# Kernel optimization log

Hardware: AMD Instinct MI355X
Metric: run time of the kernel (lower is better)

## Reference

```python
import jax, jax.numpy as jnp
import numpy as np
import math

B, S, D, H = 4, 2048, 1024, 16
DK = D // H  # 64
THETA = 10000.0


def setup_inputs() -> dict:
    key = jax.random.key(0)
    ks = jax.random.split(key, 5)
    std = 0.02
    return {
        "x": jax.random.normal(ks[0], (B, S, D), dtype=jnp.float32),
        "Wq": jax.random.normal(ks[1], (D, D), dtype=jnp.float32) * std,
        "Wk": jax.random.normal(ks[2], (D, D), dtype=jnp.float32) * std,
        "Wv": jax.random.normal(ks[3], (D, D), dtype=jnp.float32) * std,
        "Wo": jax.random.normal(ks[4], (D, D), dtype=jnp.float32) * std / math.sqrt(2 * 12),
        "token_positions": jnp.arange(S, dtype=jnp.int32),
    }


def _rope(x, pos):
    # x: [B, H, S, DK]; pos: [S]. Interleaved-pair rotary embedding.
    inv_freq = THETA ** (-jnp.arange(0, DK, 2, dtype=jnp.float32) / DK)  # [DK/2]
    ang = pos.astype(jnp.float32)[:, None] * inv_freq[None, :]  # [S, DK/2]
    cos, sin = jnp.cos(ang), jnp.sin(ang)
    x1, x2 = x[..., 0::2], x[..., 1::2]  # [B, H, S, DK/2]
    r1 = x1 * cos - x2 * sin
    r2 = x1 * sin + x2 * cos
    return jnp.stack([r1, r2], axis=-1).reshape(x.shape)


def reference(x, Wq, Wk, Wv, Wo, token_positions):
    b, s, d = x.shape
    Q = x @ Wq
    K = x @ Wk
    V = x @ Wv
    # [B, S, D] -> [B, H, S, DK]
    def split(t):
        return t.reshape(b, s, H, DK).transpose(0, 2, 1, 3)
    Qh, Kh, Vh = split(Q), split(K), split(V)
    Qh = _rope(Qh, token_positions)
    Kh = _rope(Kh, token_positions)
    scores = jnp.einsum('bhqd,bhkd->bhqk', Qh, Kh) / math.sqrt(DK)
    causal = jnp.tril(jnp.ones((s, s), dtype=bool))
    scores = jnp.where(causal, scores, -jnp.inf)
    probs = jax.nn.softmax(scores, axis=-1)
    out = jnp.einsum('bhqk,bhkd->bhqd', probs, Vh)
    out = out.transpose(0, 2, 1, 3).reshape(b, s, d)
    return out @ Wo
```

## Files before the change

### kernel.cpp

```cpp
#include <hip/hip_runtime.h>

#define B_N 4
#define S_LEN 2048
#define D_MODEL 1024
#define N_HEAD 16
#define D_HEAD 64
#define M_ROWS (B_N * S_LEN)

typedef short bf16x8 __attribute__((ext_vector_type(8)));
typedef float f32x4 __attribute__((ext_vector_type(4)));

__device__ __forceinline__ unsigned short f2bf(float f) {
  union { float f; unsigned int u; } v; v.f = f;
  unsigned int r = v.u + 0x7FFFu + ((v.u >> 16) & 1u);
  return (unsigned short)(r >> 16);
}
__device__ __forceinline__ float bf2f(unsigned short u) {
  union { unsigned int u; float f; } v; v.u = ((unsigned int)u) << 16;
  return v.f;
}
__device__ __forceinline__ bf16x8 ld8(const unsigned short* p) {
  return *reinterpret_cast<const bf16x8*>(p);
}
__device__ __forceinline__ void glds16(const unsigned short* g, unsigned short* l) {
  __builtin_amdgcn_global_load_lds(
      (const __attribute__((address_space(1))) unsigned int*)g,
      (__attribute__((address_space(3))) unsigned int*)l, 16, 0, 0);
}

__global__ __launch_bounds__(256) void rope_tab_k(const int* __restrict__ pos,
                                                  float2* __restrict__ tab) {
  const int idx = blockIdx.x * 256 + threadIdx.x;
  const int s = idx >> 5;
  const int i = idx & 31;
  const float inv = exp2f(-(float)i * 0.41524101186092029f);
  const float ang = (float)pos[s] * inv;
  tab[idx] = make_float2(cosf(ang), sinf(ang));
}

__global__ __launch_bounds__(256) void cast_k(const float* __restrict__ X,
                                              unsigned short* __restrict__ Y) {
  const size_t i = ((size_t)blockIdx.x * 256 + threadIdx.x) * 8;
  const float4 a = *reinterpret_cast<const float4*>(X + i);
  const float4 b = *reinterpret_cast<const float4*>(X + i + 4);
  __align__(16) unsigned short v[8];
  v[0] = f2bf(a.x); v[1] = f2bf(a.y); v[2] = f2bf(a.z); v[3] = f2bf(a.w);
  v[4] = f2bf(b.x); v[5] = f2bf(b.y); v[6] = f2bf(b.z); v[7] = f2bf(b.w);
  *reinterpret_cast<uint4*>(Y + i) = *reinterpret_cast<const uint4*>(v);
}

__global__ __launch_bounds__(256) void wtrans_k(
    const float* __restrict__ W0, const float* __restrict__ W1,
    const float* __restrict__ W2, const float* __restrict__ W3,
    unsigned short* __restrict__ T0, unsigned short* __restrict__ T1,
    unsigned short* __restrict__ T2, unsigned short* __restrict__ T3) {
  const int z = blockIdx.z;
  const float* __restrict__ W = (z == 0) ? W0 : (z == 1) ? W1 : (z == 2) ? W2 : W3;
  unsigned short* __restrict__ T = (z == 0) ? T0 : (z == 1) ? T1 : (z == 2) ? T2 : T3;
  __shared__ __align__(16) unsigned short tile[64][72];
  const int kb = blockIdx.x * 64;
  const int nb = blockIdx.y * 64;
#pragma unroll
  for (int it = 0; it < 2; ++it) {
    const int chunk = it * 256 + threadIdx.x;
    const int r = chunk >> 3;
    const int c8 = (chunk & 7) * 8;
    const float* src = W + (size_t)(kb + r) * D_MODEL + nb + c8;
    const float4 a = *reinterpret_cast<const float4*>(src);
    const float4 b = *reinterpret_cast<const float4*>(src + 4);
    __align__(16) unsigned short v[8];
    v[0] = f2bf(a.x); v[1] = f2bf(a.y); v[2] = f2bf(a.z); v[3] = f2bf(a.w);
    v[4] = f2bf(b.x); v[5] = f2bf(b.y); v[6] = f2bf(b.z); v[7] = f2bf(b.w);
    *reinterpret_cast<uint4*>(&tile[r][c8]) = *reinterpret_cast<const uint4*>(v);
  }
  __syncthreads();
#pragma unroll
  for (int it = 0; it < 2; ++it) {
    const int chunk = it * 256 + threadIdx.x;
    const int n = chunk >> 3;
    const int k8 = (chunk & 7) * 8;
    __align__(16) unsigned short vals[8];
#pragma unroll
    for (int j = 0; j < 8; ++j) vals[j] = tile[k8 + j][n];
    *reinterpret_cast<uint4*>(T + (size_t)(nb + n) * D_MODEL + kb + k8) =
        *reinterpret_cast<const uint4*>(vals);
  }
}

__global__ __launch_bounds__(256) void gemm2_k(
    const unsigned short* __restrict__ A, const unsigned short* __restrict__ W,
    unsigned short* __restrict__ Qo, unsigned short* __restrict__ Ko,
    unsigned short* __restrict__ VTo, float* __restrict__ OF,
    const float2* __restrict__ tab, const int mode) {
  __shared__ __align__(16) unsigned short smem[4][64][68];
  unsigned short* As = &smem[0][0][0];
  unsigned short* Bs = As + 128 * 32;

  const int tid = threadIdx.x;
  const int lane = tid & 63;
  const int w = tid >> 6;
  const int l15 = lane & 15;
  const int l4 = lane >> 4;

  const int row0 = blockIdx.x * 128;
  const int col0 = blockIdx.y * 128;

  const int srow = w * 32 + (lane >> 2);
  const int scol = (lane & 3) * 8;
  const unsigned short* ga = A + (size_t)(row0 + srow) * D_MODEL + scol;
  const unsigned short* gb = W + (size_t)(col0 + srow) * D_MODEL + scol;
  unsigned short* la = &As[(w * 32) * 32];
  unsigned short* lb = &Bs[(w * 32) * 32];

  const int wrow = (w & 1) * 64;
  const int wcol = (w >> 1) * 64;

  f32x4 acc[4][4];
  const f32x4 fz = {0.f, 0.f, 0.f, 0.f};
#pragma unroll
  for (int m = 0; m < 4; ++m)
#pragma unroll
    for (int n = 0; n < 4; ++n) acc[m][n] = fz;

  for (int kb = 0; kb < D_MODEL; kb += 32) {
    glds16(ga + kb, la);
    glds16(ga + 16 * D_MODEL + kb, la + 16 * 32);
    glds16(gb + kb, lb);
    glds16(gb + 16 * D_MODEL + kb, lb + 16 * 32);
    __syncthreads();
    bf16x8 af[4], bfr[4];
#pragma unroll
    for (int m = 0; m < 4; ++m) af[m] = ld8(&As[(wrow + m * 16 + l15) * 32 + l4 * 8]);
#pragma unroll
    for (int n = 0; n < 4; ++n) bfr[n] = ld8(&Bs[(wcol + n * 16 + l15) * 32 + l4 * 8]);
#pragma unroll
    for (int m = 0; m < 4; ++m)
#pragma unroll
      for (int n = 0; n < 4; ++n)
        acc[m][n] = __builtin_amdgcn_mfma_f32_16x16x32_bf16(af[m], bfr[n], acc[m][n], 0, 0, 0);
    __syncthreads();
  }

  if (mode == 1) {
#pragma unroll
    for (int n = 0; n < 4; ++n) {
      const int gcol = col0 + wcol + n * 16 + l15;
#pragma unroll
      for (int m = 0; m < 4; ++m)
#pragma unroll
        for (int r = 0; r < 4; ++r)
          OF[(size_t)(row0 + wrow + m * 16 + l4 * 4 + r) * D_MODEL + gcol] = acc[m][n][r];
    }
    return;
  }

  unsigned short (*T)[68] = (unsigned short(*)[68]) & smem[w];
  const bool isV = (col0 >= 2048);
  if (!isV) {
#pragma unroll
    for (int m = 0; m < 4; ++m)
#pragma unroll
      for (int n = 0; n < 4; ++n)
#pragma unroll
        for (int r = 0; r < 4; ++r)
          T[m * 16 + l4 * 4 + r][n * 16 + l15] = f2bf(acc[m][n][r]);
  } else {
#pragma unroll
    for (int m = 0; m < 4; ++m)
#pragma unroll
      for (int n = 0; n < 4; ++n)
#pragma unroll
        for (int r = 0; r < 4; ++r)
          T[n * 16 + l15][m * 16 + l4 * 4 + r] = f2bf(acc[m][n][r]);
  }

  const int lr = lane >> 3;
  const int lc = lane & 7;
  if (!isV) {
    const bool isQ = (col0 < 1024);
    unsigned short* O = isQ ? Qo : Ko;
    const float qs = isQ ? 0.18033688011112042f : 1.0f;
    const int cbase = (col0 & 1023) + wcol;
#pragma unroll
    for (int rg = 0; rg < 8; ++rg) {
      const int trow = rg * 8 + lr;
      const int grow = row0 + wrow + trow;
      const int s = grow & (S_LEN - 1);
      const bf16x8 vv = ld8(&T[trow][lc * 8]);
      const float4 tA = *reinterpret_cast<const float4*>(&tab[s * 32 + lc * 4]);
      const float4 tB = *reinterpret_cast<const float4*>(&tab[s * 32 + lc * 4 + 2]);
      float x[8];
#pragma unroll
      for (int j = 0; j < 8; ++j) x[j] = bf2f((unsigned short)vv[j]);
      __align__(16) unsigned short o8[8];
      o8[0] = f2bf((x[0] * tA.x - x[1] * tA.y) * qs);
      o8[1] = f2bf((x[0] * tA.y + x[1] * tA.x) * qs);
      o8[2] = f2bf((x[2] * tA.z - x[3] * tA.w) * qs);
      o8[3] = f2bf((x[2] * tA.w + x[3] * tA.z) * qs);
      o8[4] = f2bf((x[4] * tB.x - x[5] * tB.y) * qs);
      o8[5] = f2bf((x[4] * tB.y + x[5] * tB.x) * qs);
      o8[6] = f2bf((x[6] * tB.z - x[7] * tB.w) * qs);
      o8[7] = f2bf((x[6] * tB.w + x[7] * tB.z) * qs);
      *reinterpret_cast<uint4*>(O + (size_t)grow * D_MODEL + cbase + lc * 8) =
          *reinterpret_cast<const uint4*>(o8);
    }
  } else {
    const int vc0 = (col0 - 2048) + wcol;
    const int h = vc0 >> 6;
    const int b = row0 >> 11;
    const int s0 = (row0 & (S_LEN - 1)) + wrow;
#pragma unroll
    for (int rg = 0; rg < 8; ++rg) {
      const int dk = rg * 8 + lr;
      const bf16x8 vv = ld8(&T[dk][lc * 8]);
      *reinterpret_cast<bf16x8*>(
          VTo + ((size_t)((b << 4) + h) * 64 + dk) * S_LEN + s0 + lc * 8) = vv;
    }
  }
}

__global__ __launch_bounds__(256) void attn3_k(
    const unsigned short* __restrict__ Q, const unsigned short* __restrict__ K,
    const unsigned short* __restrict__ VT, unsigned short* __restrict__ O) {
  const int pair = blockIdx.x;
  const int h = blockIdx.y;
  const int b = blockIdx.z;
  const int tid = threadIdx.x;
  const int w = tid >> 6;
  const int lane = tid & 63;
  const int l15 = lane & 15;
  const int l4 = lane >> 4;

  __shared__ __align__(16) unsigned short Ks[64][72];
  __shared__ __align__(16) unsigned short Vs[64][72];
  __shared__ __align__(16) unsigned short Ps[4][32][72];

  const f32x4 fz = {0.f, 0.f, 0.f, 0.f};
  const unsigned short* kbase = K + (size_t)b * S_LEN * D_MODEL + h * D_HEAD;
  const unsigned short* vbase = VT + (size_t)((b << 4) + h) * 64 * S_LEN;
  const int srcl = ((lane & 15) >> 2) << 4;
  const int lq = lane & 3;

  for (int half = 0; half < 2; ++half) {
    const int qt = half ? (15 - pair) : pair;
    const int qb = qt * 128;
    const int qw0 = qb + w * 32;

    bf16x8 qf[2][2];
#pragma unroll
    for (int t = 0; t < 2; ++t)
#pragma unroll
      for (int kc = 0; kc < 2; ++kc)
        qf[t][kc] = ld8(Q + (size_t)(b * S_LEN + qw0 + t * 16 + l15) * D_MODEL +
                        h * D_HEAD + kc * 32 + l4 * 8);

    f32x4 o[4][2];
#pragma unroll
    for (int d = 0; d < 4; ++d)
#pragma unroll
      for (int t = 0; t < 2; ++t) o[d][t] = fz;
    float lsum[2][4];
#pragma unroll
    for (int t = 0; t < 2; ++t)
#pragma unroll
      for (int r = 0; r < 4; ++r) lsum[t][r] = 0.f;

    const int nkt = qb / 64 + 2;
    for (int kt = 0; kt < nkt; ++kt) {
      const int kb0 = kt * 64;
#pragma unroll
      for (int it = 0; it < 2; ++it) {
        const int chunk = it * 256 + tid;
        const int rr = chunk >> 3;
        const int c8 = (chunk & 7) * 8;
        *reinterpret_cast<uint4*>(&Ks[rr][c8]) =
            *reinterpret_cast<const uint4*>(kbase + (size_t)(kb0 + rr) * D_MODEL + c8);
        *reinterpret_cast<uint4*>(&Vs[rr][c8]) =
            *reinterpret_cast<const uint4*>(vbase + (size_t)rr * S_LEN + kb0 + c8);
      }
      __syncthreads();

      if (kb0 <= qw0 + 31) {
        bf16x8 kf[4][2];
#pragma unroll
        for (int n = 0; n < 4; ++n)
#pragma unroll
          for (int kc = 0; kc < 2; ++kc)
            kf[n][kc] = ld8(&Ks[n * 16 + l15][kc * 32 + l4 * 8]);
        f32x4 s[2][4];
#pragma unroll
        for (int t = 0; t < 2; ++t)
#pragma unroll
          for (int n = 0; n < 4; ++n) {
            f32x4 a0 = __builtin_amdgcn_mfma_f32_16x16x32_bf16(qf[t][0], kf[n][0], fz, 0, 0, 0);
            s[t][n] = __builtin_amdgcn_mfma_f32_16x16x32_bf16(qf[t][1], kf[n][1], a0, 0, 0, 0);
          }

#pragma unroll
        for (int t = 0; t < 2; ++t) {
          const bool full = (kb0 + 63 <= qw0 + t * 16);
          if (full) {
#pragma unroll
            for (int r = 0; r < 4; ++r) {
              float su = lsum[t][r];
#pragma unroll
              for (int n = 0; n < 4; ++n) {
                const float e = exp2f(s[t][n][r]);
                s[t][n][r] = e;
                su += e;
              }
              lsum[t][r] = su;
            }
          } else {
#pragma unroll
            for (int r = 0; r < 4; ++r) {
              const int q = qw0 + t * 16 + l4 * 4 + r;
              float su = lsum[t][r];
#pragma unroll
              for (int n = 0; n < 4; ++n) {
                const int key = kb0 + n * 16 + l15;
                float e = exp2f(s[t][n][r]);
                e = (key <= q) ? e : 0.f;
                s[t][n][r] = e;
                su += e;
              }
              lsum[t][r] = su;
            }
          }
#pragma unroll
          for (int r = 0; r < 4; ++r)
#pragma unroll
            for (int n = 0; n < 4; ++n)
              Ps[w][t * 16 + l4 * 4 + r][n * 16 + l15] = f2bf(s[t][n][r]);
        }

        bf16x8 vf[4][2], pf[2][2];
#pragma unroll
        for (int d = 0; d < 4; ++d)
#pragma unroll
          for (int kc = 0; kc < 2; ++kc)
            vf[d][kc] = ld8(&Vs[d * 16 + l15][kc * 32 + l4 * 8]);
#pragma unroll
        for (int t = 0; t < 2; ++t)
#pragma unroll
          for (int kc = 0; kc < 2; ++kc)
            pf[t][kc] = ld8(&Ps[w][t * 16 + l15][kc * 32 + l4 * 8]);
#pragma unroll
        for (int d = 0; d < 4; ++d)
#pragma unroll
          for (int t = 0; t < 2; ++t) {
            o[d][t] = __builtin_amdgcn_mfma_f32_16x16x32_bf16(vf[d][0], pf[t][0], o[d][t], 0, 0, 0);
            o[d][t] = __builtin_amdgcn_mfma_f32_16x16x32_bf16(vf[d][1], pf[t][1], o[d][t], 0, 0, 0);
          }
      }
      __syncthreads();
    }

#pragma unroll
    for (int t = 0; t < 2; ++t) {
#pragma unroll
      for (int dd = 1; dd < 16; dd <<= 1)
#pragma unroll
        for (int r = 0; r < 4; ++r) lsum[t][r] += __shfl_xor(lsum[t][r], dd);
      const float b0 = __shfl(lsum[t][0], srcl), b1 = __shfl(lsum[t][1], srcl);
      const float b2 = __shfl(lsum[t][2], srcl), b3 = __shfl(lsum[t][3], srcl);
      const float lv = (lq == 0) ? b0 : (lq == 1) ? b1 : (lq == 2) ? b2 : b3;
      const float li = 1.0f / lv;
      unsigned short* op = O + (size_t)(b * S_LEN + qw0 + t * 16 + l15) * D_MODEL +
                           h * D_HEAD + l4 * 4;
#pragma unroll
      for (int d = 0; d < 4; ++d) {
        ushort4 u;
        u.x = f2bf(o[d][t][0] * li); u.y = f2bf(o[d][t][1] * li);
        u.z = f2bf(o[d][t][2] * li); u.w = f2bf(o[d][t][3] * li);
        *reinterpret_cast<ushort4*>(op + d * 16) = u;
      }
    }
  }
}

extern "C" void kernel_launch(void* const* d_in, const int* in_sizes, int n_in,
                              void* d_out, int out_size, void* d_ws, size_t ws_size,
                              hipStream_t stream) {
  const float* x  = (const float*)d_in[0];
  const float* Wq = (const float*)d_in[1];
  const float* Wk = (const float*)d_in[2];
  const float* Wv = (const float*)d_in[3];
  const float* Wo = (const float*)d_in[4];
  const int* pos  = (const int*)d_in[5];
  float* out = (float*)d_out;

  char* ws = (char*)d_ws;
  const size_t big = (size_t)M_ROWS * D_MODEL * 2;
  const size_t wsz = (size_t)D_MODEL * D_MODEL * 2;
  unsigned short* xb  = (unsigned short*)(ws + 0 * big);
  unsigned short* Qb  = (unsigned short*)(ws + 1 * big);
  unsigned short* Kb  = (unsigned short*)(ws + 2 * big);
  unsigned short* VT  = (unsigned short*)(ws + 3 * big);
  unsigned short* Wqkvt = (unsigned short*)(ws + 4 * big);
  unsigned short* Wot   = (unsigned short*)(ws + 4 * big + 3 * wsz);
  float2* tab = (float2*)d_out;

  rope_tab_k<<<dim3(S_LEN * 32 / 256), 256, 0, stream>>>(pos, tab);
  cast_k<<<dim3(M_ROWS * D_MODEL / 2048), 256, 0, stream>>>(x, xb);
  wtrans_k<<<dim3(16, 16, 4), 256, 0, stream>>>(
      Wq, Wk, Wv, Wo, Wqkvt, Wqkvt + (size_t)D_MODEL * D_MODEL,
      Wqkvt + 2 * (size_t)D_MODEL * D_MODEL, Wot);
  gemm2_k<<<dim3(M_ROWS / 128, 3 * D_MODEL / 128), 256, 0, stream>>>(
      xb, Wqkvt, Qb, Kb, VT, nullptr, tab, 0);
  attn3_k<<<dim3(8, N_HEAD, B_N), 256, 0, stream>>>(Qb, Kb, VT, Qb);
  gemm2_k<<<dim3(M_ROWS / 128, D_MODEL / 128), 256, 0, stream>>>(
      Qb, Wot, nullptr, nullptr, nullptr, out, nullptr, 1);
}
```

Measured before the change: 296.6 us.

## Keep attention probabilities in registers and prefetch K/V tiles

The attention kernel computes S transposed (K as the A operand), so each lane holds four consecutive keys for one query row. Those probabilities are packed directly into bf16x4 operands for 16x16x16 MFMA, which removes the per-wave LDS round trip for P and shrinks the row-sum reduction to two shuffles. K/V tiles for the next step are now prefetched into registers while the current tile is computed. Float-to-bf16 conversions everywhere switch to the packed hardware intrinsic. The cost is more register pressure, and the smaller MFMA shape issues more instructions.

```diff
diff --git a/kernel.cpp b/kernel.cpp
--- a/kernel.cpp
+++ b/kernel.cpp
@@ -1,4 +1,5 @@
 #include <hip/hip_runtime.h>
+#include <hip/hip_bf16.h>
 
 #define B_N 4
 #define S_LEN 2048
@@ -8,7 +9,14 @@
 #define M_ROWS (B_N * S_LEN)
 
 typedef short bf16x8 __attribute__((ext_vector_type(8)));
+typedef short bf16x4 __attribute__((ext_vector_type(4)));
 typedef float f32x4 __attribute__((ext_vector_type(4)));
+
+#if __has_builtin(__builtin_amdgcn_mfma_f32_16x16x16bf16_1k)
+#define HAVE_MFMA16 1
+#else
+#define HAVE_MFMA16 0
+#endif
 
 __device__ __forceinline__ unsigned short f2bf(float f) {
   union { float f; unsigned int u; } v; v.f = f;
@@ -19,8 +27,16 @@
   union { unsigned int u; float f; } v; v.u = ((unsigned int)u) << 16;
   return v.f;
 }
+__device__ __forceinline__ unsigned int pkbf(float a, float b) {
+  union { __hip_bfloat162 h; unsigned int u; } cv;
+  cv.h = __float22bfloat162_rn(make_float2(a, b));
+  return cv.u;
+}
 __device__ __forceinline__ bf16x8 ld8(const unsigned short* p) {
   return *reinterpret_cast<const bf16x8*>(p);
+}
+__device__ __forceinline__ bf16x4 ld4(const unsigned short* p) {
+  return *reinterpret_cast<const bf16x4*>(p);
 }
 __device__ __forceinline__ void glds16(const unsigned short* g, unsigned short* l) {
   __builtin_amdgcn_global_load_lds(
@@ -43,10 +59,10 @@
   const size_t i = ((size_t)blockIdx.x * 256 + threadIdx.x) * 8;
   const float4 a = *reinterpret_cast<const float4*>(X + i);
   const float4 b = *reinterpret_cast<const float4*>(X + i + 4);
-  __align__(16) unsigned short v[8];
-  v[0] = f2bf(a.x); v[1] = f2bf(a.y); v[2] = f2bf(a.z); v[3] = f2bf(a.w);
-  v[4] = f2bf(b.x); v[5] = f2bf(b.y); v[6] = f2bf(b.z); v[7] = f2bf(b.w);
-  *reinterpret_cast<uint4*>(Y + i) = *reinterpret_cast<const uint4*>(v);
+  union { unsigned int u[4]; uint4 v; } o;
+  o.u[0] = pkbf(a.x, a.y); o.u[1] = pkbf(a.z, a.w);
+  o.u[2] = pkbf(b.x, b.y); o.u[3] = pkbf(b.z, b.w);
+  *reinterpret_cast<uint4*>(Y + i) = o.v;
 }
 
 __global__ __launch_bounds__(256) void wtrans_k(
@@ -68,10 +84,10 @@
     const float* src = W + (size_t)(kb + r) * D_MODEL + nb + c8;
     const float4 a = *reinterpret_cast<const float4*>(src);
     const float4 b = *reinterpret_cast<const float4*>(src + 4);
-    __align__(16) unsigned short v[8];
-    v[0] = f2bf(a.x); v[1] = f2bf(a.y); v[2] = f2bf(a.z); v[3] = f2bf(a.w);
-    v[4] = f2bf(b.x); v[5] = f2bf(b.y); v[6] = f2bf(b.z); v[7] = f2bf(b.w);
-    *reinterpret_cast<uint4*>(&tile[r][c8]) = *reinterpret_cast<const uint4*>(v);
+    union { unsigned int u[4]; uint4 v; } o;
+    o.u[0] = pkbf(a.x, a.y); o.u[1] = pkbf(a.z, a.w);
+    o.u[2] = pkbf(b.x, b.y); o.u[3] = pkbf(b.z, b.w);
+    *reinterpret_cast<uint4*>(&tile[r][c8]) = o.v;
   }
   __syncthreads();
 #pragma unroll
@@ -192,17 +208,12 @@
       float x[8];
 #pragma unroll
       for (int j = 0; j < 8; ++j) x[j] = bf2f((unsigned short)vv[j]);
-      __align__(16) unsigned short o8[8];
-      o8[0] = f2bf((x[0] * tA.x - x[1] * tA.y) * qs);
-      o8[1] = f2bf((x[0] * tA.y + x[1] * tA.x) * qs);
-      o8[2] = f2bf((x[2] * tA.z - x[3] * tA.w) * qs);
-      o8[3] = f2bf((x[2] * tA.w + x[3] * tA.z) * qs);
-      o8[4] = f2bf((x[4] * tB.x - x[5] * tB.y) * qs);
-      o8[5] = f2bf((x[4] * tB.y + x[5] * tB.x) * qs);
-      o8[6] = f2bf((x[6] * tB.z - x[7] * tB.w) * qs);
-      o8[7] = f2bf((x[6] * tB.w + x[7] * tB.z) * qs);
-      *reinterpret_cast<uint4*>(O + (size_t)grow * D_MODEL + cbase + lc * 8) =
-          *reinterpret_cast<const uint4*>(o8);
+      union { unsigned int u[4]; uint4 v; } o;
+      o.u[0] = pkbf((x[0] * tA.x - x[1] * tA.y) * qs, (x[0] * tA.y + x[1] * tA.x) * qs);
+      o.u[1] = pkbf((x[2] * tA.z - x[3] * tA.w) * qs, (x[2] * tA.w + x[3] * tA.z) * qs);
+      o.u[2] = pkbf((x[4] * tB.x - x[5] * tB.y) * qs, (x[4] * tB.y + x[5] * tB.x) * qs);
+      o.u[3] = pkbf((x[6] * tB.z - x[7] * tB.w) * qs, (x[6] * tB.w + x[7] * tB.z) * qs);
+      *reinterpret_cast<uint4*>(O + (size_t)grow * D_MODEL + cbase + lc * 8) = o.v;
     }
   } else {
     const int vc0 = (col0 - 2048) + wcol;
@@ -219,7 +230,7 @@
   }
 }
 
-__global__ __launch_bounds__(256) void attn3_k(
+__global__ __launch_bounds__(256) void attn4_k(
     const unsigned short* __restrict__ Q, const unsigned short* __restrict__ K,
     const unsigned short* __restrict__ VT, unsigned short* __restrict__ O) {
   const int pair = blockIdx.x;
@@ -233,13 +244,16 @@
 
   __shared__ __align__(16) unsigned short Ks[64][72];
   __shared__ __align__(16) unsigned short Vs[64][72];
+#if !HAVE_MFMA16
   __shared__ __align__(16) unsigned short Ps[4][32][72];
+#endif
 
   const f32x4 fz = {0.f, 0.f, 0.f, 0.f};
   const unsigned short* kbase = K + (size_t)b * S_LEN * D_MODEL + h * D_HEAD;
   const unsigned short* vbase = VT + (size_t)((b << 4) + h) * 64 * S_LEN;
-  const int srcl = ((lane & 15) >> 2) << 4;
-  const int lq = lane & 3;
+
+  const int rr = tid >> 3;
+  const int c8 = (tid & 7) * 8;
 
   for (int half = 0; half < 2; ++half) {
     const int qt = half ? (15 - pair) : pair;
@@ -259,26 +273,32 @@
     for (int d = 0; d < 4; ++d)
 #pragma unroll
       for (int t = 0; t < 2; ++t) o[d][t] = fz;
-    float lsum[2][4];
-#pragma unroll
-    for (int t = 0; t < 2; ++t)
-#pragma unroll
-      for (int r = 0; r < 4; ++r) lsum[t][r] = 0.f;
+    float lsum[2] = {0.f, 0.f};
 
     const int nkt = qb / 64 + 2;
+    uint4 kreg[2], vreg[2];
+#pragma unroll
+    for (int it = 0; it < 2; ++it) {
+      kreg[it] = *reinterpret_cast<const uint4*>(kbase + (size_t)(rr + it * 32) * D_MODEL + c8);
+      vreg[it] = *reinterpret_cast<const uint4*>(vbase + (size_t)(rr + it * 32) * S_LEN + c8);
+    }
+
     for (int kt = 0; kt < nkt; ++kt) {
       const int kb0 = kt * 64;
 #pragma unroll
       for (int it = 0; it < 2; ++it) {
-        const int chunk = it * 256 + tid;
-        const int rr = chunk >> 3;
-        const int c8 = (chunk & 7) * 8;
-        *reinterpret_cast<uint4*>(&Ks[rr][c8]) =
-            *reinterpret_cast<const uint4*>(kbase + (size_t)(kb0 + rr) * D_MODEL + c8);
-        *reinterpret_cast<uint4*>(&Vs[rr][c8]) =
-            *reinterpret_cast<const uint4*>(vbase + (size_t)rr * S_LEN + kb0 + c8);
+        *reinterpret_cast<uint4*>(&Ks[rr + it * 32][c8]) = kreg[it];
+        *reinterpret_cast<uint4*>(&Vs[rr + it * 32][c8]) = vreg[it];
       }
       __syncthreads();
+      if (kt + 1 < nkt) {
+        const int nb0 = kb0 + 64;
+#pragma unroll
+        for (int it = 0; it < 2; ++it) {
+          kreg[it] = *reinterpret_cast<const uint4*>(kbase + (size_t)(nb0 + rr + it * 32) * D_MODEL + c8);
+          vreg[it] = *reinterpret_cast<const uint4*>(vbase + (size_t)(rr + it * 32) * S_LEN + nb0 + c8);
+        }
+      }
 
       if (kb0 <= qw0 + 31) {
         bf16x8 kf[4][2];
@@ -292,88 +312,94 @@
         for (int t = 0; t < 2; ++t)
 #pragma unroll
           for (int n = 0; n < 4; ++n) {
-            f32x4 a0 = __builtin_amdgcn_mfma_f32_16x16x32_bf16(qf[t][0], kf[n][0], fz, 0, 0, 0);
-            s[t][n] = __builtin_amdgcn_mfma_f32_16x16x32_bf16(qf[t][1], kf[n][1], a0, 0, 0, 0);
+            f32x4 a0 = __builtin_amdgcn_mfma_f32_16x16x32_bf16(kf[n][0], qf[t][0], fz, 0, 0, 0);
+            s[t][n] = __builtin_amdgcn_mfma_f32_16x16x32_bf16(kf[n][1], qf[t][1], a0, 0, 0, 0);
           }
 
+        bf16x4 pf[2][4];
 #pragma unroll
         for (int t = 0; t < 2; ++t) {
           const bool full = (kb0 + 63 <= qw0 + t * 16);
-          if (full) {
-#pragma unroll
-            for (int r = 0; r < 4; ++r) {
-              float su = lsum[t][r];
-#pragma unroll
-              for (int n = 0; n < 4; ++n) {
-                const float e = exp2f(s[t][n][r]);
-                s[t][n][r] = e;
-                su += e;
+          const int q = qw0 + t * 16 + l15;
+          float su = lsum[t];
+#pragma unroll
+          for (int n = 0; n < 4; ++n) {
+            float e[4];
+            if (full) {
+#pragma unroll
+              for (int r = 0; r < 4; ++r) e[r] = exp2f(s[t][n][r]);
+            } else {
+#pragma unroll
+              for (int r = 0; r < 4; ++r) {
+                const int key = kb0 + n * 16 + l4 * 4 + r;
+                const float v = exp2f(s[t][n][r]);
+                e[r] = (key <= q) ? v : 0.f;
               }
-              lsum[t][r] = su;
             }
-          } else {
-#pragma unroll
-            for (int r = 0; r < 4; ++r) {
-              const int q = qw0 + t * 16 + l4 * 4 + r;
-              float su = lsum[t][r];
-#pragma unroll
-              for (int n = 0; n < 4; ++n) {
-                const int key = kb0 + n * 16 + l15;
-                float e = exp2f(s[t][n][r]);
-                e = (key <= q) ? e : 0.f;
-                s[t][n][r] = e;
-                su += e;
-              }
-              lsum[t][r] = su;
-            }
+            su += (e[0] + e[1]) + (e[2] + e[3]);
+            union { unsigned int u[2]; bf16x4 v; } pk;
+            pk.u[0] = pkbf(e[0], e[1]);
+            pk.u[1] = pkbf(e[2], e[3]);
+            pf[t][n] = pk.v;
           }
-#pragma unroll
-          for (int r = 0; r < 4; ++r)
-#pragma unroll
-            for (int n = 0; n < 4; ++n)
-              Ps[w][t * 16 + l4 * 4 + r][n * 16 + l15] = f2bf(s[t][n][r]);
+          lsum[t] = su;
         }
 
-        bf16x8 vf[4][2], pf[2][2];
+#if HAVE_MFMA16
+#pragma unroll
+        for (int d = 0; d < 4; ++d) {
+          bf16x4 vfc[4];
+#pragma unroll
+          for (int c = 0; c < 4; ++c) vfc[c] = ld4(&Vs[d * 16 + l15][c * 16 + l4 * 4]);
+#pragma unroll
+          for (int t = 0; t < 2; ++t)
+#pragma unroll
+            for (int c = 0; c < 4; ++c)
+              o[d][t] = __builtin_amdgcn_mfma_f32_16x16x16bf16_1k(vfc[c], pf[t][c], o[d][t], 0, 0, 0);
+        }
+#else
+#pragma unroll
+        for (int t = 0; t < 2; ++t)
+#pragma unroll
+          for (int n = 0; n < 4; ++n)
+            *reinterpret_cast<bf16x4*>(&Ps[w][t * 16 + l15][n * 16 + l4 * 4]) = pf[t][n];
+        bf16x8 pfr[2][2], vf8[4][2];
+#pragma unroll
+        for (int t = 0; t < 2; ++t)
+#pragma unroll
+          for (int kc = 0; kc < 2; ++kc)
+            pfr[t][kc] = ld8(&Ps[w][t * 16 + l15][kc * 32 + l4 * 8]);
 #pragma unroll
         for (int d = 0; d < 4; ++d)
 #pragma unroll
           for (int kc = 0; kc < 2; ++kc)
-            vf[d][kc] = ld8(&Vs[d * 16 + l15][kc * 32 + l4 * 8]);
-#pragma unroll
-        for (int t = 0; t < 2; ++t)
-#pragma unroll
-          for (int kc = 0; kc < 2; ++kc)
-            pf[t][kc] = ld8(&Ps[w][t * 16 + l15][kc * 32 + l4 * 8]);
+            vf8[d][kc] = ld8(&Vs[d * 16 + l15][kc * 32 + l4 * 8]);
 #pragma unroll
         for (int d = 0; d < 4; ++d)
 #pragma unroll
           for (int t = 0; t < 2; ++t) {
-            o[d][t] = __builtin_amdgcn_mfma_f32_16x16x32_bf16(vf[d][0], pf[t][0], o[d][t], 0, 0, 0);
-            o[d][t] = __builtin_amdgcn_mfma_f32_16x16x32_bf16(vf[d][1], pf[t][1], o[d][t], 0, 0, 0);
+            o[d][t] = __builtin_amdgcn_mfma_f32_16x16x32_bf16(vf8[d][0], pfr[t][0], o[d][t], 0, 0, 0);
+            o[d][t] = __builtin_amdgcn_mfma_f32_16x16x32_bf16(vf8[d][1], pfr[t][1], o[d][t], 0, 0, 0);
           }
+#endif
       }
       __syncthreads();
     }
 
 #pragma unroll
     for (int t = 0; t < 2; ++t) {
-#pragma unroll
-      for (int dd = 1; dd < 16; dd <<= 1)
-#pragma unroll
-        for (int r = 0; r < 4; ++r) lsum[t][r] += __shfl_xor(lsum[t][r], dd);
-      const float b0 = __shfl(lsum[t][0], srcl), b1 = __shfl(lsum[t][1], srcl);
-      const float b2 = __shfl(lsum[t][2], srcl), b3 = __shfl(lsum[t][3], srcl);
-      const float lv = (lq == 0) ? b0 : (lq == 1) ? b1 : (lq == 2) ? b2 : b3;
-      const float li = 1.0f / lv;
+      float s = lsum[t];
+      s += __shfl_xor(s, 16);
+      s += __shfl_xor(s, 32);
+      const float li = 1.0f / s;
       unsigned short* op = O + (size_t)(b * S_LEN + qw0 + t * 16 + l15) * D_MODEL +
                            h * D_HEAD + l4 * 4;
 #pragma unroll
       for (int d = 0; d < 4; ++d) {
-        ushort4 u;
-        u.x = f2bf(o[d][t][0] * li); u.y = f2bf(o[d][t][1] * li);
-        u.z = f2bf(o[d][t][2] * li); u.w = f2bf(o[d][t][3] * li);
-        *reinterpret_cast<ushort4*>(op + d * 16) = u;
+        union { unsigned int u[2]; uint2 v; } ov;
+        ov.u[0] = pkbf(o[d][t][0] * li, o[d][t][1] * li);
+        ov.u[1] = pkbf(o[d][t][2] * li, o[d][t][3] * li);
+        *reinterpret_cast<uint2*>(op + d * 16) = ov.v;
       }
     }
   }
@@ -408,7 +434,7 @@
       Wqkvt + 2 * (size_t)D_MODEL * D_MODEL, Wot);
   gemm2_k<<<dim3(M_ROWS / 128, 3 * D_MODEL / 128), 256, 0, stream>>>(
       xb, Wqkvt, Qb, Kb, VT, nullptr, tab, 0);
-  attn3_k<<<dim3(8, N_HEAD, B_N), 256, 0, stream>>>(Qb, Kb, VT, Qb);
+  attn4_k<<<dim3(8, N_HEAD, B_N), 256, 0, stream>>>(Qb, Kb, VT, Qb);
   gemm2_k<<<dim3(M_ROWS / 128, D_MODEL / 128), 256, 0, stream>>>(
       Qb, Wot, nullptr, nullptr, nullptr, out, nullptr, 1);
 }
```

Result: slower. 326.1 us (+10.0%).
